# Kernel optimization log

Measured on AMD Instinct MI355X. Metric: run time of the kernel, lower is better.

Reference implementation:

```python
import jax, jax.numpy as jnp
import numpy as np

S_N, B, K, D = 5, 2048, 128, 64
STU, EXE = 100000, 20000
H1, H2 = 256, 128


def setup_inputs() -> dict:
    key = jax.random.key(0)
    ks = jax.random.split(key, 40)
    f = jax.random.normal
    u = jax.random.uniform
    inp = {
        'stu_id': jax.random.randint(ks[0], (B,), 0, STU),
        'exer_id': jax.random.randint(ks[1], (B,), 0, EXE),
        'kn_r': (u(ks[2], (B, K)) < 0.3).astype(jnp.float32),
        'stu_cnt': u(ks[3], (STU, 1)) * 50.0,
        'exer_cnt': u(ks[4], (EXE, 1)) * 50.0,
        'student_mean_emb': f(ks[5], (STU, D)) * 0.1,
        'exercise_mean_emb': f(ks[6], (EXE, D)) * 0.1,
        'knowledge_mean_emb': f(ks[7], (K, D)) * 0.1,
        'e_disc_mean': f(ks[8], (EXE, 1)) * 0.1,
        'e_disc_std_eta': u(ks[9], (EXE, 1), minval=-4.0, maxval=0.0),
        'stat_mean_w': f(ks[10], (1, D)) * 0.1, 'stat_mean_b': jnp.zeros((1,)),
        'stat_std_w': f(ks[11], (1, D)) * 0.1, 'stat_std_b': jnp.zeros((1,)),
        'kdiff_mean_w': f(ks[12], (1, D)) * 0.1, 'kdiff_mean_b': jnp.zeros((1,)),
        'kdiff_std_w': f(ks[13], (1, D)) * 0.1, 'kdiff_std_b': jnp.zeros((1,)),
        'lam1_stu': jnp.ones((1,)), 'lam2_stu': jnp.ones((1,)),
        'lam1_exer': jnp.ones((1,)), 'lam2_exer': jnp.ones((1,)),
        # BayesPosLinear params; w_mu initialized as log|xavier| -> negative values
        'w_mu1': f(ks[14], (H1, K)) * 0.5 - 3.0,
        'w_std_eta1': u(ks[15], (H1, K), minval=-4.0, maxval=0.0),
        'b_mu1': f(ks[16], (H1,)) * 0.05, 'b_std_eta1': f(ks[17], (H1,)) * 0.05,
        'w_mu2': f(ks[18], (H2, H1)) * 0.5 - 3.0,
        'w_std_eta2': u(ks[19], (H2, H1), minval=-4.0, maxval=0.0),
        'b_mu2': f(ks[20], (H2,)) * 0.05, 'b_std_eta2': f(ks[21], (H2,)) * 0.05,
        'w_mu3': f(ks[22], (1, H2)) * 0.5 - 3.0,
        'w_std_eta3': u(ks[23], (1, H2), minval=-4.0, maxval=0.0),
        'b_mu3': f(ks[24], (1,)) * 0.05, 'b_std_eta3': f(ks[25], (1,)) * 0.05,
        # reparameterization noise (generated once for determinism)
        'eps_stat': f(ks[26], (S_N, B, K)),
        'eps_kdiff': f(ks[27], (S_N, B, K)),
        'eps_disc': f(ks[28], (S_N, B, 1)),
        'eps_w1': f(ks[29], (B, H1, K)), 'eps_b1': f(ks[30], (B, H1)),
        'eps_w2': f(ks[31], (B, H2, H1)), 'eps_b2': f(ks[32], (B, H2)),
        'eps_w3': f(ks[33], (B, 1, H2)), 'eps_b3': f(ks[34], (B, 1)),
    }
    return inp


def _kl_std_normal(mu, std):
    # KL( N(mu, std) || N(0,1) )
    return -jnp.log(std) + 0.5 * (std * std + mu * mu - 1.0)


def _bpl(x, w_mu, w_std_eta, b_mu, b_std_eta, eps_w, eps_b):
    # BayesPosLinear.forward (training): per-batch-element sampled positive weights.
    sp = jax.nn.softplus
    std_w = 1e-6 + sp(w_std_eta)                      # [O,I]
    std_b = 1e-6 + sp(b_std_eta)                      # [O]
    w = jnp.exp(w_mu[None] + std_w[None] * eps_w)     # [B,O,I]
    b = b_mu[None] + std_b[None] * eps_b              # [B,O]
    # vectorized replacement for the python loop of F.linear over batch
    out = jnp.einsum('sbi,boi->sbo', x, w) + b[None]  # [S,B,O]
    kl = _kl_std_normal(w_mu, std_w).sum() + _kl_std_normal(b_mu, std_b).sum()
    return out, kl


def reference(stu_id, exer_id, kn_r, stu_cnt, exer_cnt,
              student_mean_emb, exercise_mean_emb, knowledge_mean_emb,
              e_disc_mean, e_disc_std_eta,
              stat_mean_w, stat_mean_b, stat_std_w, stat_std_b,
              kdiff_mean_w, kdiff_mean_b, kdiff_std_w, kdiff_std_b,
              lam1_stu, lam2_stu, lam1_exer, lam2_exer,
              w_mu1, w_std_eta1, b_mu1, b_std_eta1,
              w_mu2, w_std_eta2, b_mu2, b_std_eta2,
              w_mu3, w_std_eta3, b_mu3, b_std_eta3,
              eps_stat, eps_kdiff, eps_disc,
              eps_w1, eps_b1, eps_w2, eps_b2, eps_w3, eps_b3):
    sp = jax.nn.softplus
    su = student_mean_emb[stu_id]                         # [B,D]
    ee = exercise_mean_emb[exer_id]                       # [B,D]
    ps = su[:, None, :] * knowledge_mean_emb[None]        # [B,K,D] gmf interaction
    stat_mean = jnp.einsum('bkd,d->bk', ps, stat_mean_w[0]) + stat_mean_b[0]
    stat_std_model = sp(jnp.einsum('bkd,d->bk', ps, stat_std_w[0]) + stat_std_b[0])
    stat_std_data = sp(lam1_stu) * jnp.exp(-sp(lam2_stu) * stu_cnt[stu_id])   # [B,1]
    stat_std = stat_std_data + stat_std_model             # combine_method '+'

    pe = ee[:, None, :] * knowledge_mean_emb[None]        # [B,K,D]
    kdiff_mean = jnp.einsum('bkd,d->bk', pe, kdiff_mean_w[0]) + kdiff_mean_b[0]
    kdiff_std_model = sp(jnp.einsum('bkd,d->bk', pe, kdiff_std_w[0]) + kdiff_std_b[0])
    kdiff_std_data = sp(lam1_exer) * jnp.exp(-sp(lam2_exer) * exer_cnt[exer_id])
    kdiff_std = kdiff_std_data + kdiff_std_model

    # reparameterized samples, sample_n copies
    stat = jax.nn.sigmoid(stat_mean[None] + stat_std[None] * eps_stat)        # [S,B,K]
    kdiff = jax.nn.sigmoid(kdiff_mean[None] + kdiff_std[None] * eps_kdiff)    # [S,B,K]
    disc = jax.nn.sigmoid(e_disc_mean[exer_id][None]
                          + sp(e_disc_std_eta[exer_id])[None] * eps_disc)     # [S,B,1]

    x = disc * (stat - kdiff) * kn_r[None]                # [S,B,K]
    h, kl1 = _bpl(x, w_mu1, w_std_eta1, b_mu1, b_std_eta1, eps_w1, eps_b1)
    h = jnp.tanh(h)  # interaction_activation; dropout omitted (eval-equivalent)
    h, kl2 = _bpl(h, w_mu2, w_std_eta2, b_mu2, b_std_eta2, eps_w2, eps_b2)
    h = jnp.tanh(h)
    o, kl3 = _bpl(h, w_mu3, w_std_eta3, b_mu3, b_std_eta3, eps_w3, eps_b3)
    out = jax.nn.sigmoid(o)                               # [S,B,1]
    return out, kl1 + kl2 + kl3
```

## Files before the change

### kernel.cpp

```cpp
#include <hip/hip_runtime.h>

#define SN 5
#define BB 2048
#define KK 128
#define DD 64
#define H1 256
#define H2 128

#define W3S   65536
#define S3S   65664
#define SB1F  65792
#define SB2F  66048
#define SB3F  66176
#define N_PREP 16897

#define LOG2E 1.4426950408889634f

#if defined(__has_builtin)
#if __has_builtin(__builtin_amdgcn_exp2f)
#define EXP2(x) __builtin_amdgcn_exp2f(x)
#else
#define EXP2(x) __expf(0.6931471805599453f * (x))
#endif
#if __has_builtin(__builtin_amdgcn_rcpf)
#define RCP(x) __builtin_amdgcn_rcpf(x)
#else
#define RCP(x) (1.0f / (x))
#endif
#else
#define EXP2(x) __expf(0.6931471805599453f * (x))
#define RCP(x) (1.0f / (x))
#endif

__device__ __forceinline__ void bar_lgkm() {
  asm volatile("s_waitcnt lgkmcnt(0)\n\ts_barrier" ::: "memory");
}

__device__ __forceinline__ float sp_(float x) {
  return (x > 20.f) ? x : log1pf(__expf(x));
}
__device__ __forceinline__ float sig_(float x) { return RCP(1.f + __expf(-x)); }
__device__ __forceinline__ float tanh_fast(float x) {
  float e = EXP2(2.8853900817779268f * x);
  return 1.f - 2.f * RCP(e + 1.f);
}
__device__ __forceinline__ float4 exp2m4_(float4 m, float4 s, float4 e) {
  float4 r;
  r.x = EXP2(m.x + s.x * e.x);
  r.y = EXP2(m.y + s.y * e.y);
  r.z = EXP2(m.z + s.z * e.z);
  r.w = EXP2(m.w + s.w * e.w);
  return r;
}
__device__ __forceinline__ float dot4_(float4 a, float4 b) {
  return a.x * b.x + a.y * b.y + a.z * b.z + a.w * b.w;
}
__device__ __forceinline__ unsigned int pb_(float x) {
  unsigned int u = __float_as_uint(x);
  return (u + 0x7fffu + ((u >> 16) & 1u)) >> 16;
}
__device__ __forceinline__ void unpk_(float4 pk, float4& m, float4& s) {
  unsigned int u0 = __float_as_uint(pk.x), u1 = __float_as_uint(pk.y);
  unsigned int u2 = __float_as_uint(pk.z), u3 = __float_as_uint(pk.w);
  m.x = __uint_as_float(u0 << 16); m.y = __uint_as_float(u0 & 0xffff0000u);
  m.z = __uint_as_float(u1 << 16); m.w = __uint_as_float(u1 & 0xffff0000u);
  s.x = __uint_as_float(u2 << 16); s.y = __uint_as_float(u2 & 0xffff0000u);
  s.z = __uint_as_float(u3 << 16); s.w = __uint_as_float(u3 & 0xffff0000u);
}

__global__ __launch_bounds__(256) void prep_kl(
    const float* w_mu1, const float* eta_w1, const float* b_mu1, const float* eta_b1,
    const float* w_mu2, const float* eta_w2, const float* b_mu2, const float* eta_b2,
    const float* w_mu3, const float* eta_w3, const float* b_mu3, const float* eta_b3,
    float* ws, float* kl_out)
{
  int f = blockIdx.x * 256 + threadIdx.x;
  float kle = 0.f;
  if (f < 16384) {
    const float* mup; const float* etp; int q; int outq;
    if (f < 8192) { mup = w_mu1; etp = eta_w1; q = f; outq = f; }
    else          { mup = w_mu2; etp = eta_w2; q = f - 8192; outq = f; }
    float4 mu = ((const float4*)mup)[q];
    float4 et = ((const float4*)etp)[q];
    float4 sd;
    sd.x = 1e-6f + sp_(et.x); sd.y = 1e-6f + sp_(et.y);
    sd.z = 1e-6f + sp_(et.z); sd.w = 1e-6f + sp_(et.w);
    kle = (-logf(sd.x) + 0.5f * (sd.x * sd.x + mu.x * mu.x - 1.f))
        + (-logf(sd.y) + 0.5f * (sd.y * sd.y + mu.y * mu.y - 1.f))
        + (-logf(sd.z) + 0.5f * (sd.z * sd.z + mu.z * mu.z - 1.f))
        + (-logf(sd.w) + 0.5f * (sd.w * sd.w + mu.w * mu.w - 1.f));
    uint4 pk;
    pk.x = pb_(mu.x * LOG2E) | (pb_(mu.y * LOG2E) << 16);
    pk.y = pb_(mu.z * LOG2E) | (pb_(mu.w * LOG2E) << 16);
    pk.z = pb_(sd.x * LOG2E) | (pb_(sd.y * LOG2E) << 16);
    pk.w = pb_(sd.z * LOG2E) | (pb_(sd.w * LOG2E) << 16);
    ((uint4*)ws)[outq] = pk;
  } else if (f < N_PREP) {
    float m, s;
    if (f < 16512) {
      int i = f - 16384;
      m = w_mu3[i]; s = 1e-6f + sp_(eta_w3[i]);
      ws[W3S + i] = m * LOG2E;
      ws[S3S + i] = s * LOG2E;
    } else if (f < 16768) {
      int i = f - 16512;
      m = b_mu1[i]; s = 1e-6f + sp_(eta_b1[i]);
      ws[SB1F + i] = s;
    } else if (f < 16896) {
      int i = f - 16768;
      m = b_mu2[i]; s = 1e-6f + sp_(eta_b2[i]);
      ws[SB2F + i] = s;
    } else {
      m = b_mu3[0]; s = 1e-6f + sp_(eta_b3[0]);
      ws[SB3F] = s;
    }
    kle = -logf(s) + 0.5f * (s * s + m * m - 1.0f);
  }
  __shared__ float red[256];
  red[threadIdx.x] = kle;
  __syncthreads();
  for (int w = 128; w > 0; w >>= 1) {
    if (threadIdx.x < w) red[threadIdx.x] += red[threadIdx.x + w];
    __syncthreads();
  }
  if (threadIdx.x == 0) atomicAdd(kl_out, red[0]);
}

__global__ __launch_bounds__(256) void bayes_main(
    const int* __restrict__ stu_id, const int* __restrict__ exer_id,
    const float* __restrict__ kn_r,
    const float* __restrict__ stu_cnt, const float* __restrict__ exer_cnt,
    const float* __restrict__ s_emb, const float* __restrict__ e_emb,
    const float* __restrict__ k_emb,
    const float* __restrict__ e_disc_mean, const float* __restrict__ e_disc_eta,
    const float* __restrict__ w_sm, const float* __restrict__ b_sm,
    const float* __restrict__ w_ss, const float* __restrict__ b_ss,
    const float* __restrict__ w_km, const float* __restrict__ b_km,
    const float* __restrict__ w_ks, const float* __restrict__ b_ks,
    const float* __restrict__ lam1s, const float* __restrict__ lam2s,
    const float* __restrict__ lam1e, const float* __restrict__ lam2e,
    const float* __restrict__ b_mu1, const float* __restrict__ b_mu2,
    const float* __restrict__ b_mu3,
    const float* __restrict__ eps_stat, const float* __restrict__ eps_kdiff,
    const float* __restrict__ eps_disc,
    const float* __restrict__ eps_w1, const float* __restrict__ eps_b1,
    const float* __restrict__ eps_w2, const float* __restrict__ eps_b2,
    const float* __restrict__ eps_w3, const float* __restrict__ eps_b3,
    const float* __restrict__ tabs,
    float* __restrict__ out)
{
  const int b0 = blockIdx.x * 2;
  const int t = threadIdx.x;
  const int g = t >> 4, l16 = t & 15;

  __shared__ __align__(16) float cmb[2][4][DD];
  __shared__ float smean[2][KK], sstd[2][KK], kmean[2][KK], kstd[2][KK];
  __shared__ float discs[2][8];
  __shared__ __align__(16) float xs[2][SN][KK];
  __shared__ __align__(16) float h1s[2][SN][H1];
  __shared__ __align__(16) float h2s[2][SN][H2];
  __shared__ float bias1[2][H1];
  __shared__ float bias2[2][H2];
  __shared__ float w3v[2][H2];

  const int stu0 = stu_id[b0], ex0 = exer_id[b0];
  const int stu1 = stu_id[b0 + 1], ex1 = exer_id[b0 + 1];

  {
    const int sel = t >> 6, d = t & 63;
    if (sel == 0) {
      float sv = s_emb[(size_t)stu0 * DD + d];
      cmb[0][0][d] = sv * w_sm[d]; cmb[0][1][d] = sv * w_ss[d];
    } else if (sel == 1) {
      float ev = e_emb[(size_t)ex0 * DD + d];
      cmb[0][2][d] = ev * w_km[d]; cmb[0][3][d] = ev * w_ks[d];
    } else if (sel == 2) {
      float sv = s_emb[(size_t)stu1 * DD + d];
      cmb[1][0][d] = sv * w_sm[d]; cmb[1][1][d] = sv * w_ss[d];
    } else {
      float ev = e_emb[(size_t)ex1 * DD + d];
      cmb[1][2][d] = ev * w_km[d]; cmb[1][3][d] = ev * w_ks[d];
    }
  }
  {
    float sb1 = tabs[SB1F + t], bm1 = b_mu1[t];
    bias1[0][t] = bm1 + sb1 * eps_b1[(size_t)b0 * H1 + t];
    bias1[1][t] = bm1 + sb1 * eps_b1[(size_t)(b0 + 1) * H1 + t];
  }
  if (t < H2) {
    float sb2 = tabs[SB2F + t], bm2 = b_mu2[t];
    bias2[0][t] = bm2 + sb2 * eps_b2[(size_t)b0 * H2 + t];
    bias2[1][t] = bm2 + sb2 * eps_b2[(size_t)(b0 + 1) * H2 + t];
    float w3m = tabs[W3S + t], w3s = tabs[S3S + t];
    w3v[0][t] = EXP2(w3m + w3s * eps_w3[(size_t)b0 * H2 + t]);
    w3v[1][t] = EXP2(w3m + w3s * eps_w3[(size_t)(b0 + 1) * H2 + t]);
  }
  if (t < 16) {
    int ib = t >> 3, s = t & 7;
    if (s < SN) {
      int exx = ib ? ex1 : ex0;
      float de = sp_(e_disc_eta[exx]);
      discs[ib][s] = sig_(e_disc_mean[exx] + de * eps_disc[(size_t)s * BB + b0 + ib]);
    }
  }
  bar_lgkm();

  {
    const int k = t & 127, half = t >> 7;
    const float4* kr4 = (const float4*)(k_emb + (size_t)k * DD);
    const float4* cA0 = (const float4*)cmb[0][half ? 2 : 0];
    const float4* cB0 = (const float4*)cmb[0][half ? 3 : 1];
    const float4* cA1 = (const float4*)cmb[1][half ? 2 : 0];
    const float4* cB1 = (const float4*)cmb[1][half ? 3 : 1];
    float am0 = 0.f, as0 = 0.f, am1 = 0.f, as1 = 0.f;
    #pragma unroll
    for (int j = 0; j < DD / 4; ++j) {
      float4 kv = kr4[j];
      am0 += dot4_(kv, cA0[j]);
      as0 += dot4_(kv, cB0[j]);
      am1 += dot4_(kv, cA1[j]);
      as1 += dot4_(kv, cB1[j]);
    }
    if (half == 0) {
      float l1 = sp_(lam1s[0]), l2 = sp_(lam2s[0]);
      float sd0 = l1 * __expf(-l2 * stu_cnt[stu0]);
      float sd1 = l1 * __expf(-l2 * stu_cnt[stu1]);
      smean[0][k] = am0 + b_sm[0];  sstd[0][k] = sd0 + sp_(as0 + b_ss[0]);
      smean[1][k] = am1 + b_sm[0];  sstd[1][k] = sd1 + sp_(as1 + b_ss[0]);
    } else {
      float l1 = sp_(lam1e[0]), l2 = sp_(lam2e[0]);
      float ed0 = l1 * __expf(-l2 * exer_cnt[ex0]);
      float ed1 = l1 * __expf(-l2 * exer_cnt[ex1]);
      kmean[0][k] = am0 + b_km[0];  kstd[0][k] = ed0 + sp_(as0 + b_ks[0]);
      kmean[1][k] = am1 + b_km[0];  kstd[1][k] = ed1 + sp_(as1 + b_ks[0]);
    }
  }

  const int lane1 = g * 32 + l16;
  const float4* ep1a = (const float4*)(eps_w1 + (size_t)b0 * H1 * KK) + lane1;
  const float4* ep1b = ep1a + 8192;
  const float4* pk1 = (const float4*)tabs;
  float4 cA0 = ep1a[0], cA1 = ep1a[16], cA2 = ep1a[512], cA3 = ep1a[528];
  float4 cB0 = ep1b[0], cB1 = ep1b[16], cB2 = ep1b[512], cB3 = ep1b[528];
  float4 pq0 = pk1[lane1], pq1 = pk1[lane1 + 16];
  float4 pq2 = pk1[lane1 + 512], pq3 = pk1[lane1 + 528];

  bar_lgkm();

  {
    const int k = t & 127, ib = t >> 7;
    const int b = b0 + ib;
    float knr = kn_r[(size_t)b * KK + k];
    float sm = smean[ib][k], ss = sstd[ib][k], km = kmean[ib][k], ks = kstd[ib][k];
    #pragma unroll
    for (int s = 0; s < SN; ++s) {
      float es = eps_stat [((size_t)s * BB + b) * KK + k];
      float ek = eps_kdiff[((size_t)s * BB + b) * KK + k];
      xs[ib][s][k] = discs[ib][s] * (sig_(sm + ss * es) - sig_(km + ks * ek)) * knr;
    }
  }
  bar_lgkm();

  {
    #pragma unroll
    for (int p = 0; p < 8; ++p) {
      const int B0 = p * 1024;
      float4 nA0, nA1, nA2, nA3, nB0, nB1, nB2, nB3, nq0, nq1, nq2, nq3;
      if (p < 7) {
        nA0 = ep1a[B0 + 1024]; nA1 = ep1a[B0 + 1040];
        nA2 = ep1a[B0 + 1536]; nA3 = ep1a[B0 + 1552];
        nB0 = ep1b[B0 + 1024]; nB1 = ep1b[B0 + 1040];
        nB2 = ep1b[B0 + 1536]; nB3 = ep1b[B0 + 1552];
        nq0 = pk1[B0 + 1024 + lane1]; nq1 = pk1[B0 + 1040 + lane1];
        nq2 = pk1[B0 + 1536 + lane1]; nq3 = pk1[B0 + 1552 + lane1];
      }
      float4 m0, s0, m1, s1, m2, s2v, m3, s3;
      unpk_(pq0, m0, s0); unpk_(pq1, m1, s1);
      unpk_(pq2, m2, s2v); unpk_(pq3, m3, s3);
      const int o0 = p * 32 + g, o1 = o0 + 16;

      #pragma unroll
      for (int ib = 0; ib < 2; ++ib) {
        float4 e0 = ib ? cB0 : cA0;
        float4 e1 = ib ? cB1 : cA1;
        float4 e2 = ib ? cB2 : cA2;
        float4 e3 = ib ? cB3 : cA3;
        float4 wA0 = exp2m4_(m0, s0, e0);
        float4 wA1 = exp2m4_(m1, s1, e1);
        float4 wB0 = exp2m4_(m2, s2v, e2);
        float4 wB1 = exp2m4_(m3, s3, e3);
        float red[SN];
        #pragma unroll
        for (int s2 = 0; s2 < SN; ++s2) {
          float4 xa = *(const float4*)&xs[ib][s2][l16 * 4];
          float4 xb = *(const float4*)&xs[ib][s2][64 + l16 * 4];
          float a0 = dot4_(wA0, xa) + dot4_(wA1, xb);
          float a1 = dot4_(wB0, xa) + dot4_(wB1, xb);
          float u0 = __shfl_xor(a0, 8);
          float u1 = __shfl_xor(a1, 8);
          float a = (l16 < 8) ? (a0 + u0) : (a1 + u1);
          a += __shfl_xor(a, 4);
          a += __shfl_xor(a, 2);
          a += __shfl_xor(a, 1);
          red[s2] = a;
        }
        if (l16 == 0) {
          #pragma unroll
          for (int s2 = 0; s2 < SN; ++s2) h1s[ib][s2][o0] = tanh_fast(red[s2] + bias1[ib][o0]);
        } else if (l16 == 8) {
          #pragma unroll
          for (int s2 = 0; s2 < SN; ++s2) h1s[ib][s2][o1] = tanh_fast(red[s2] + bias1[ib][o1]);
        }
      }
      cA0 = nA0; cA1 = nA1; cA2 = nA2; cA3 = nA3;
      cB0 = nB0; cB1 = nB1; cB2 = nB2; cB3 = nB3;
      pq0 = nq0; pq1 = nq1; pq2 = nq2; pq3 = nq3;
    }
  }

  const int lane2 = g * 64 + l16;
  const float4* ep2a = (const float4*)(eps_w2 + (size_t)b0 * H2 * H1) + lane2;
  const float4* ep2b = ep2a + 8192;
  const float4* pk2 = (const float4*)tabs + 8192;
  float4 fA0 = ep2a[0], fA1 = ep2a[16], fA2 = ep2a[32], fA3 = ep2a[48];
  float4 fB0 = ep2b[0], fB1 = ep2b[16], fB2 = ep2b[32], fB3 = ep2b[48];
  float4 rq0 = pk2[lane2], rq1 = pk2[lane2 + 16];
  float4 rq2 = pk2[lane2 + 32], rq3 = pk2[lane2 + 48];

  bar_lgkm();

  {
    #pragma unroll
    for (int p = 0; p < 8; ++p) {
      const int B0 = p * 1024;
      float4 nA0, nA1, nA2, nA3, nB0, nB1, nB2, nB3, nq0, nq1, nq2, nq3;
      if (p < 7) {
        nA0 = ep2a[B0 + 1024]; nA1 = ep2a[B0 + 1040];
        nA2 = ep2a[B0 + 1056]; nA3 = ep2a[B0 + 1072];
        nB0 = ep2b[B0 + 1024]; nB1 = ep2b[B0 + 1040];
        nB2 = ep2b[B0 + 1056]; nB3 = ep2b[B0 + 1072];
        nq0 = pk2[B0 + 1024 + lane2]; nq1 = pk2[B0 + 1040 + lane2];
        nq2 = pk2[B0 + 1056 + lane2]; nq3 = pk2[B0 + 1072 + lane2];
      }
      float4 m0, s0, m1, s1, m2, s2v, m3, s3;
      unpk_(rq0, m0, s0); unpk_(rq1, m1, s1);
      unpk_(rq2, m2, s2v); unpk_(rq3, m3, s3);
      const int o = p * 16 + g;

      #pragma unroll
      for (int ib = 0; ib < 2; ++ib) {
        float4 e0 = ib ? fB0 : fA0;
        float4 e1 = ib ? fB1 : fA1;
        float4 e2 = ib ? fB2 : fA2;
        float4 e3 = ib ? fB3 : fA3;
        float4 w0 = exp2m4_(m0, s0, e0);
        float4 w1 = exp2m4_(m1, s1, e1);
        float4 w2 = exp2m4_(m2, s2v, e2);
        float4 w3 = exp2m4_(m3, s3, e3);
        float red[SN];
        #pragma unroll
        for (int s2 = 0; s2 < SN; ++s2) {
          float4 ha = *(const float4*)&h1s[ib][s2][l16 * 4];
          float4 hb = *(const float4*)&h1s[ib][s2][64 + l16 * 4];
          float4 hc = *(const float4*)&h1s[ib][s2][128 + l16 * 4];
          float4 hd = *(const float4*)&h1s[ib][s2][192 + l16 * 4];
          float a = dot4_(w0, ha) + dot4_(w1, hb) + dot4_(w2, hc) + dot4_(w3, hd);
          a += __shfl_xor(a, 8);
          a += __shfl_xor(a, 4);
          a += __shfl_xor(a, 2);
          a += __shfl_xor(a, 1);
          red[s2] = a;
        }
        if (l16 == 0) {
          #pragma unroll
          for (int s2 = 0; s2 < SN; ++s2) h2s[ib][s2][o] = tanh_fast(red[s2] + bias2[ib][o]);
        }
      }
      fA0 = nA0; fA1 = nA1; fA2 = nA2; fA3 = nA3;
      fB0 = nB0; fB1 = nB1; fB2 = nB2; fB3 = nB3;
      rq0 = nq0; rq1 = nq1; rq2 = nq2; rq3 = nq3;
    }
  }
  bar_lgkm();

  if (t < 128) {
    const int ib = t >> 6, l = t & 63;
    const int b = b0 + ib;
    float w3a = w3v[ib][l];
    float w3b = w3v[ib][l + 64];
    float part[SN];
    #pragma unroll
    for (int s2 = 0; s2 < SN; ++s2) part[s2] = w3a * h2s[ib][s2][l] + w3b * h2s[ib][s2][l + 64];
    #pragma unroll
    for (int off = 32; off >= 1; off >>= 1) {
      #pragma unroll
      for (int s2 = 0; s2 < SN; ++s2) part[s2] += __shfl_xor(part[s2], off);
    }
    if (l == 0) {
      float bb3 = b_mu3[0] + tabs[SB3F] * eps_b3[b];
      #pragma unroll
      for (int s2 = 0; s2 < SN; ++s2) out[(size_t)s2 * BB + b] = sig_(part[s2] + bb3);
    }
  }
}

extern "C" void kernel_launch(void* const* d_in, const int* in_sizes, int n_in,
                              void* d_out, int out_size, void* d_ws, size_t ws_size,
                              hipStream_t stream) {
  const int*   stu_id      = (const int*)  d_in[0];
  const int*   exer_id     = (const int*)  d_in[1];
  const float* kn_r        = (const float*)d_in[2];
  const float* stu_cnt     = (const float*)d_in[3];
  const float* exer_cnt    = (const float*)d_in[4];
  const float* s_emb       = (const float*)d_in[5];
  const float* e_emb       = (const float*)d_in[6];
  const float* k_emb       = (const float*)d_in[7];
  const float* e_disc_mean = (const float*)d_in[8];
  const float* e_disc_eta  = (const float*)d_in[9];
  const float* w_sm        = (const float*)d_in[10];
  const float* b_sm        = (const float*)d_in[11];
  const float* w_ss        = (const float*)d_in[12];
  const float* b_ss        = (const float*)d_in[13];
  const float* w_km        = (const float*)d_in[14];
  const float* b_km        = (const float*)d_in[15];
  const float* w_ks        = (const float*)d_in[16];
  const float* b_ks        = (const float*)d_in[17];
  const float* lam1s       = (const float*)d_in[18];
  const float* lam2s       = (const float*)d_in[19];
  const float* lam1e       = (const float*)d_in[20];
  const float* lam2e       = (const float*)d_in[21];
  const float* w_mu1       = (const float*)d_in[22];
  const float* eta_w1      = (const float*)d_in[23];
  const float* b_mu1       = (const float*)d_in[24];
  const float* eta_b1      = (const float*)d_in[25];
  const float* w_mu2       = (const float*)d_in[26];
  const float* eta_w2      = (const float*)d_in[27];
  const float* b_mu2       = (const float*)d_in[28];
  const float* eta_b2      = (const float*)d_in[29];
  const float* w_mu3       = (const float*)d_in[30];
  const float* eta_w3      = (const float*)d_in[31];
  const float* b_mu3       = (const float*)d_in[32];
  const float* eta_b3      = (const float*)d_in[33];
  const float* eps_stat    = (const float*)d_in[34];
  const float* eps_kdiff   = (const float*)d_in[35];
  const float* eps_disc    = (const float*)d_in[36];
  const float* eps_w1      = (const float*)d_in[37];
  const float* eps_b1      = (const float*)d_in[38];
  const float* eps_w2      = (const float*)d_in[39];
  const float* eps_b2      = (const float*)d_in[40];
  const float* eps_w3      = (const float*)d_in[41];
  const float* eps_b3      = (const float*)d_in[42];

  float* out = (float*)d_out;
  float* ws  = (float*)d_ws;

  hipMemsetAsync((char*)d_out + (size_t)SN * BB * sizeof(float), 0, sizeof(float), stream);

  prep_kl<<<(N_PREP + 255) / 256, 256, 0, stream>>>(
      w_mu1, eta_w1, b_mu1, eta_b1,
      w_mu2, eta_w2, b_mu2, eta_b2,
      w_mu3, eta_w3, b_mu3, eta_b3,
      ws, out + (size_t)SN * BB);

  bayes_main<<<BB / 2, 256, 0, stream>>>(
      stu_id, exer_id, kn_r, stu_cnt, exer_cnt,
      s_emb, e_emb, k_emb, e_disc_mean, e_disc_eta,
      w_sm, b_sm, w_ss, b_ss, w_km, b_km, w_ks, b_ks,
      lam1s, lam2s, lam1e, lam2e,
      b_mu1, b_mu2, b_mu3,
      eps_stat, eps_kdiff, eps_disc,
      eps_w1, eps_b1, eps_w2, eps_b2, eps_w3, eps_b3,
      ws, out);
}
```

Before: 125.0 us.

## Process four batch rows per block and drop manual register prefetch of eps

Each block now handles four batch elements instead of two, so the per-layer packed weight mean/std tables are loaded and unpacked once per four rows rather than once per two, and the grid is halved. The hand-written software prefetch of the next eps_w1/eps_w2 tile and packed weights is removed; loads are now issued inline and the compiler is left to schedule them. This doubles shared memory per block and raises register pressure, which may lower occupancy, and latency hiding of the large eps streams now depends on the compiler.

Result: slower. 134.3 us (+7.4%).

```diff
diff --git a/kernel.cpp b/kernel.cpp
--- a/kernel.cpp
+++ b/kernel.cpp
@@ -77,9 +77,9 @@
   int f = blockIdx.x * 256 + threadIdx.x;
   float kle = 0.f;
   if (f < 16384) {
-    const float* mup; const float* etp; int q; int outq;
-    if (f < 8192) { mup = w_mu1; etp = eta_w1; q = f; outq = f; }
-    else          { mup = w_mu2; etp = eta_w2; q = f - 8192; outq = f; }
+    const float* mup; const float* etp; int q;
+    if (f < 8192) { mup = w_mu1; etp = eta_w1; q = f; }
+    else          { mup = w_mu2; etp = eta_w2; q = f - 8192; }
     float4 mu = ((const float4*)mup)[q];
     float4 et = ((const float4*)etp)[q];
     float4 sd;
@@ -94,7 +94,7 @@
     pk.y = pb_(mu.z * LOG2E) | (pb_(mu.w * LOG2E) << 16);
     pk.z = pb_(sd.x * LOG2E) | (pb_(sd.y * LOG2E) << 16);
     pk.w = pb_(sd.z * LOG2E) | (pb_(sd.w * LOG2E) << 16);
-    ((uint4*)ws)[outq] = pk;
+    ((uint4*)ws)[f] = pk;
   } else if (f < N_PREP) {
     float m, s;
     if (f < 16512) {
@@ -149,56 +149,47 @@
     const float* __restrict__ tabs,
     float* __restrict__ out)
 {
-  const int b0 = blockIdx.x * 2;
+  const int b0 = blockIdx.x * 4;
   const int t = threadIdx.x;
   const int g = t >> 4, l16 = t & 15;
 
-  __shared__ __align__(16) float cmb[2][4][DD];
-  __shared__ float smean[2][KK], sstd[2][KK], kmean[2][KK], kstd[2][KK];
-  __shared__ float discs[2][8];
-  __shared__ __align__(16) float xs[2][SN][KK];
-  __shared__ __align__(16) float h1s[2][SN][H1];
-  __shared__ __align__(16) float h2s[2][SN][H2];
-  __shared__ float bias1[2][H1];
-  __shared__ float bias2[2][H2];
-  __shared__ float w3v[2][H2];
-
-  const int stu0 = stu_id[b0], ex0 = exer_id[b0];
-  const int stu1 = stu_id[b0 + 1], ex1 = exer_id[b0 + 1];
-
-  {
-    const int sel = t >> 6, d = t & 63;
-    if (sel == 0) {
-      float sv = s_emb[(size_t)stu0 * DD + d];
-      cmb[0][0][d] = sv * w_sm[d]; cmb[0][1][d] = sv * w_ss[d];
-    } else if (sel == 1) {
-      float ev = e_emb[(size_t)ex0 * DD + d];
-      cmb[0][2][d] = ev * w_km[d]; cmb[0][3][d] = ev * w_ks[d];
-    } else if (sel == 2) {
-      float sv = s_emb[(size_t)stu1 * DD + d];
-      cmb[1][0][d] = sv * w_sm[d]; cmb[1][1][d] = sv * w_ss[d];
-    } else {
-      float ev = e_emb[(size_t)ex1 * DD + d];
-      cmb[1][2][d] = ev * w_km[d]; cmb[1][3][d] = ev * w_ks[d];
-    }
+  __shared__ __align__(16) float cmb[4][4][DD];
+  __shared__ float smean[4][KK], sstd[4][KK], kmean[4][KK], kstd[4][KK];
+  __shared__ float discs[4][8];
+  __shared__ __align__(16) float xs[4][SN][KK];
+  __shared__ __align__(16) float h1s[4][SN][H1];
+  __shared__ __align__(16) float h2s[4][SN][H2];
+  __shared__ float bias1[4][H1];
+  __shared__ float bias2[4][H2];
+  __shared__ float w3v[4][H2];
+
+  {
+    const int ib = t >> 6, d = t & 63;
+    const int stu = stu_id[b0 + ib], ex = exer_id[b0 + ib];
+    float sv = s_emb[(size_t)stu * DD + d];
+    float ev = e_emb[(size_t)ex * DD + d];
+    cmb[ib][0][d] = sv * w_sm[d]; cmb[ib][1][d] = sv * w_ss[d];
+    cmb[ib][2][d] = ev * w_km[d]; cmb[ib][3][d] = ev * w_ks[d];
   }
   {
     float sb1 = tabs[SB1F + t], bm1 = b_mu1[t];
-    bias1[0][t] = bm1 + sb1 * eps_b1[(size_t)b0 * H1 + t];
-    bias1[1][t] = bm1 + sb1 * eps_b1[(size_t)(b0 + 1) * H1 + t];
+    #pragma unroll
+    for (int ib = 0; ib < 4; ++ib)
+      bias1[ib][t] = bm1 + sb1 * eps_b1[(size_t)(b0 + ib) * H1 + t];
   }
   if (t < H2) {
     float sb2 = tabs[SB2F + t], bm2 = b_mu2[t];
-    bias2[0][t] = bm2 + sb2 * eps_b2[(size_t)b0 * H2 + t];
-    bias2[1][t] = bm2 + sb2 * eps_b2[(size_t)(b0 + 1) * H2 + t];
     float w3m = tabs[W3S + t], w3s = tabs[S3S + t];
-    w3v[0][t] = EXP2(w3m + w3s * eps_w3[(size_t)b0 * H2 + t]);
-    w3v[1][t] = EXP2(w3m + w3s * eps_w3[(size_t)(b0 + 1) * H2 + t]);
-  }
-  if (t < 16) {
+    #pragma unroll
+    for (int ib = 0; ib < 4; ++ib) {
+      bias2[ib][t] = bm2 + sb2 * eps_b2[(size_t)(b0 + ib) * H2 + t];
+      w3v[ib][t] = EXP2(w3m + w3s * eps_w3[(size_t)(b0 + ib) * H2 + t]);
+    }
+  }
+  if (t < 32) {
     int ib = t >> 3, s = t & 7;
     if (s < SN) {
-      int exx = ib ? ex1 : ex0;
+      int exx = exer_id[b0 + ib];
       float de = sp_(e_disc_eta[exx]);
       discs[ib][s] = sig_(e_disc_mean[exx] + de * eps_disc[(size_t)s * BB + b0 + ib]);
     }
@@ -208,83 +199,74 @@
   {
     const int k = t & 127, half = t >> 7;
     const float4* kr4 = (const float4*)(k_emb + (size_t)k * DD);
-    const float4* cA0 = (const float4*)cmb[0][half ? 2 : 0];
-    const float4* cB0 = (const float4*)cmb[0][half ? 3 : 1];
-    const float4* cA1 = (const float4*)cmb[1][half ? 2 : 0];
-    const float4* cB1 = (const float4*)cmb[1][half ? 3 : 1];
-    float am0 = 0.f, as0 = 0.f, am1 = 0.f, as1 = 0.f;
+    float am[4] = {0.f, 0.f, 0.f, 0.f}, asv[4] = {0.f, 0.f, 0.f, 0.f};
     #pragma unroll
     for (int j = 0; j < DD / 4; ++j) {
       float4 kv = kr4[j];
-      am0 += dot4_(kv, cA0[j]);
-      as0 += dot4_(kv, cB0[j]);
-      am1 += dot4_(kv, cA1[j]);
-      as1 += dot4_(kv, cB1[j]);
+      #pragma unroll
+      for (int ib = 0; ib < 4; ++ib) {
+        const float4* cA = (const float4*)cmb[ib][half ? 2 : 0];
+        const float4* cB = (const float4*)cmb[ib][half ? 3 : 1];
+        am[ib]  += dot4_(kv, cA[j]);
+        asv[ib] += dot4_(kv, cB[j]);
+      }
     }
     if (half == 0) {
       float l1 = sp_(lam1s[0]), l2 = sp_(lam2s[0]);
-      float sd0 = l1 * __expf(-l2 * stu_cnt[stu0]);
-      float sd1 = l1 * __expf(-l2 * stu_cnt[stu1]);
-      smean[0][k] = am0 + b_sm[0];  sstd[0][k] = sd0 + sp_(as0 + b_ss[0]);
-      smean[1][k] = am1 + b_sm[0];  sstd[1][k] = sd1 + sp_(as1 + b_ss[0]);
+      #pragma unroll
+      for (int ib = 0; ib < 4; ++ib) {
+        float sd = l1 * __expf(-l2 * stu_cnt[stu_id[b0 + ib]]);
+        smean[ib][k] = am[ib] + b_sm[0];
+        sstd[ib][k]  = sd + sp_(asv[ib] + b_ss[0]);
+      }
     } else {
       float l1 = sp_(lam1e[0]), l2 = sp_(lam2e[0]);
-      float ed0 = l1 * __expf(-l2 * exer_cnt[ex0]);
-      float ed1 = l1 * __expf(-l2 * exer_cnt[ex1]);
-      kmean[0][k] = am0 + b_km[0];  kstd[0][k] = ed0 + sp_(as0 + b_ks[0]);
-      kmean[1][k] = am1 + b_km[0];  kstd[1][k] = ed1 + sp_(as1 + b_ks[0]);
-    }
-  }
-
-  const int lane1 = g * 32 + l16;
-  const float4* ep1a = (const float4*)(eps_w1 + (size_t)b0 * H1 * KK) + lane1;
-  const float4* ep1b = ep1a + 8192;
-  const float4* pk1 = (const float4*)tabs;
-  float4 cA0 = ep1a[0], cA1 = ep1a[16], cA2 = ep1a[512], cA3 = ep1a[528];
-  float4 cB0 = ep1b[0], cB1 = ep1b[16], cB2 = ep1b[512], cB3 = ep1b[528];
-  float4 pq0 = pk1[lane1], pq1 = pk1[lane1 + 16];
-  float4 pq2 = pk1[lane1 + 512], pq3 = pk1[lane1 + 528];
-
+      #pragma unroll
+      for (int ib = 0; ib < 4; ++ib) {
+        float ed = l1 * __expf(-l2 * exer_cnt[exer_id[b0 + ib]]);
+        kmean[ib][k] = am[ib] + b_km[0];
+        kstd[ib][k]  = ed + sp_(asv[ib] + b_ks[0]);
+      }
+    }
+  }
   bar_lgkm();
 
   {
-    const int k = t & 127, ib = t >> 7;
-    const int b = b0 + ib;
-    float knr = kn_r[(size_t)b * KK + k];
-    float sm = smean[ib][k], ss = sstd[ib][k], km = kmean[ib][k], ks = kstd[ib][k];
-    #pragma unroll
-    for (int s = 0; s < SN; ++s) {
-      float es = eps_stat [((size_t)s * BB + b) * KK + k];
-      float ek = eps_kdiff[((size_t)s * BB + b) * KK + k];
-      xs[ib][s][k] = discs[ib][s] * (sig_(sm + ss * es) - sig_(km + ks * ek)) * knr;
+    const int k = t & 127, ih = t >> 7;
+    #pragma unroll
+    for (int v = 0; v < 2; ++v) {
+      const int ib = ih + 2 * v;
+      const int b = b0 + ib;
+      float knr = kn_r[(size_t)b * KK + k];
+      float sm = smean[ib][k], ss = sstd[ib][k], km = kmean[ib][k], ks = kstd[ib][k];
+      #pragma unroll
+      for (int s = 0; s < SN; ++s) {
+        float es = eps_stat [((size_t)s * BB + b) * KK + k];
+        float ek = eps_kdiff[((size_t)s * BB + b) * KK + k];
+        xs[ib][s][k] = discs[ib][s] * (sig_(sm + ss * es) - sig_(km + ks * ek)) * knr;
+      }
     }
   }
   bar_lgkm();
 
   {
+    const int lane1 = g * 32 + l16;
+    const float4* eb1 = (const float4*)(eps_w1 + (size_t)b0 * H1 * KK) + lane1;
+    const float4* pk1 = (const float4*)tabs;
     #pragma unroll
     for (int p = 0; p < 8; ++p) {
       const int B0 = p * 1024;
-      float4 nA0, nA1, nA2, nA3, nB0, nB1, nB2, nB3, nq0, nq1, nq2, nq3;
-      if (p < 7) {
-        nA0 = ep1a[B0 + 1024]; nA1 = ep1a[B0 + 1040];
-        nA2 = ep1a[B0 + 1536]; nA3 = ep1a[B0 + 1552];
-        nB0 = ep1b[B0 + 1024]; nB1 = ep1b[B0 + 1040];
-        nB2 = ep1b[B0 + 1536]; nB3 = ep1b[B0 + 1552];
-        nq0 = pk1[B0 + 1024 + lane1]; nq1 = pk1[B0 + 1040 + lane1];
-        nq2 = pk1[B0 + 1536 + lane1]; nq3 = pk1[B0 + 1552 + lane1];
-      }
+      float4 pq0 = pk1[B0 + lane1],       pq1 = pk1[B0 + 16 + lane1];
+      float4 pq2 = pk1[B0 + 512 + lane1], pq3 = pk1[B0 + 528 + lane1];
       float4 m0, s0, m1, s1, m2, s2v, m3, s3;
       unpk_(pq0, m0, s0); unpk_(pq1, m1, s1);
       unpk_(pq2, m2, s2v); unpk_(pq3, m3, s3);
       const int o0 = p * 32 + g, o1 = o0 + 16;
 
       #pragma unroll
-      for (int ib = 0; ib < 2; ++ib) {
-        float4 e0 = ib ? cB0 : cA0;
-        float4 e1 = ib ? cB1 : cA1;
-        float4 e2 = ib ? cB2 : cA2;
-        float4 e3 = ib ? cB3 : cA3;
+      for (int ib = 0; ib < 4; ++ib) {
+        const float4* ep = eb1 + (size_t)ib * 8192;
+        float4 e0 = ep[B0], e1 = ep[B0 + 16], e2 = ep[B0 + 512], e3 = ep[B0 + 528];
         float4 wA0 = exp2m4_(m0, s0, e0);
         float4 wA1 = exp2m4_(m1, s1, e1);
         float4 wB0 = exp2m4_(m2, s2v, e2);
@@ -312,47 +294,28 @@
           for (int s2 = 0; s2 < SN; ++s2) h1s[ib][s2][o1] = tanh_fast(red[s2] + bias1[ib][o1]);
         }
       }
-      cA0 = nA0; cA1 = nA1; cA2 = nA2; cA3 = nA3;
-      cB0 = nB0; cB1 = nB1; cB2 = nB2; cB3 = nB3;
-      pq0 = nq0; pq1 = nq1; pq2 = nq2; pq3 = nq3;
-    }
-  }
-
-  const int lane2 = g * 64 + l16;
-  const float4* ep2a = (const float4*)(eps_w2 + (size_t)b0 * H2 * H1) + lane2;
-  const float4* ep2b = ep2a + 8192;
-  const float4* pk2 = (const float4*)tabs + 8192;
-  float4 fA0 = ep2a[0], fA1 = ep2a[16], fA2 = ep2a[32], fA3 = ep2a[48];
-  float4 fB0 = ep2b[0], fB1 = ep2b[16], fB2 = ep2b[32], fB3 = ep2b[48];
-  float4 rq0 = pk2[lane2], rq1 = pk2[lane2 + 16];
-  float4 rq2 = pk2[lane2 + 32], rq3 = pk2[lane2 + 48];
-
+    }
+  }
   bar_lgkm();
 
   {
+    const int lane2 = g * 64 + l16;
+    const float4* eb2 = (const float4*)(eps_w2 + (size_t)b0 * H2 * H1) + lane2;
+    const float4* pk2 = (const float4*)tabs + 8192;
     #pragma unroll
     for (int p = 0; p < 8; ++p) {
       const int B0 = p * 1024;
-      float4 nA0, nA1, nA2, nA3, nB0, nB1, nB2, nB3, nq0, nq1, nq2, nq3;
-      if (p < 7) {
-        nA0 = ep2a[B0 + 1024]; nA1 = ep2a[B0 + 1040];
-        nA2 = ep2a[B0 + 1056]; nA3 = ep2a[B0 + 1072];
-        nB0 = ep2b[B0 + 1024]; nB1 = ep2b[B0 + 1040];
-        nB2 = ep2b[B0 + 1056]; nB3 = ep2b[B0 + 1072];
-        nq0 = pk2[B0 + 1024 + lane2]; nq1 = pk2[B0 + 1040 + lane2];
-        nq2 = pk2[B0 + 1056 + lane2]; nq3 = pk2[B0 + 1072 + lane2];
-      }
+      float4 rq0 = pk2[B0 + lane2],      rq1 = pk2[B0 + 16 + lane2];
+      float4 rq2 = pk2[B0 + 32 + lane2], rq3 = pk2[B0 + 48 + lane2];
       float4 m0, s0, m1, s1, m2, s2v, m3, s3;
       unpk_(rq0, m0, s0); unpk_(rq1, m1, s1);
       unpk_(rq2, m2, s2v); unpk_(rq3, m3, s3);
       const int o = p * 16 + g;
 
       #pragma unroll
-      for (int ib = 0; ib < 2; ++ib) {
-        float4 e0 = ib ? fB0 : fA0;
-        float4 e1 = ib ? fB1 : fA1;
-        float4 e2 = ib ? fB2 : fA2;
-        float4 e3 = ib ? fB3 : fA3;
+      for (int ib = 0; ib < 4; ++ib) {
+        const float4* ep = eb2 + (size_t)ib * 8192;
+        float4 e0 = ep[B0], e1 = ep[B0 + 16], e2 = ep[B0 + 32], e3 = ep[B0 + 48];
         float4 w0 = exp2m4_(m0, s0, e0);
         float4 w1 = exp2m4_(m1, s1, e1);
         float4 w2 = exp2m4_(m2, s2v, e2);
@@ -376,14 +339,11 @@
           for (int s2 = 0; s2 < SN; ++s2) h2s[ib][s2][o] = tanh_fast(red[s2] + bias2[ib][o]);
         }
       }
-      fA0 = nA0; fA1 = nA1; fA2 = nA2; fA3 = nA3;
-      fB0 = nB0; fB1 = nB1; fB2 = nB2; fB3 = nB3;
-      rq0 = nq0; rq1 = nq1; rq2 = nq2; rq3 = nq3;
     }
   }
   bar_lgkm();
 
-  if (t < 128) {
+  {
     const int ib = t >> 6, l = t & 63;
     const int b = b0 + ib;
     float w3a = w3v[ib][l];
@@ -462,7 +422,7 @@
       w_mu3, eta_w3, b_mu3, eta_b3,
       ws, out + (size_t)SN * BB);
 
-  bayes_main<<<BB / 2, 256, 0, stream>>>(
+  bayes_main<<<BB / 4, 256, 0, stream>>>(
       stu_id, exer_id, kn_r, stu_cnt, exer_cnt,
       s_emb, e_emb, k_emb, e_disc_mean, e_disc_eta,
       w_sm, b_sm, w_ss, b_ss, w_km, b_km, w_ks, b_ks,
```
